# Kernel optimization log

Hardware: AMD Instinct MI355X
Metric: run time of the kernel (lower is better)

## Reference

```python
import jax, jax.numpy as jnp
import numpy as np
import math

FEATURE_DIM = 128
CLASS_NUM = 10000
BATCH = 4096


def setup_inputs() -> dict:
    key = jax.random.key(0)
    k1, k2, k3 = jax.random.split(key, 3)
    # feat scaled by 0.1 so squared distances are O(1) and exp(-d/1.8) is non-degenerate
    feat = jax.random.normal(k1, (BATCH, FEATURE_DIM), dtype=jnp.float32) * 0.1
    # xavier_uniform over [class_num, feature_dim]
    bound = math.sqrt(6.0 / (CLASS_NUM + FEATURE_DIM))
    weights = jax.random.uniform(k2, (CLASS_NUM, FEATURE_DIM), dtype=jnp.float32,
                                 minval=-bound, maxval=bound)
    label = jax.random.randint(k3, (BATCH,), 0, CLASS_NUM, dtype=jnp.int64)
    return {"feat": feat, "weights": weights, "label": label}


def reference(feat, weights, label):
    # pairwise squared euclidean distance via GEMM trick (avoids [B,C,D] diff tensor)
    f2 = jnp.sum(feat * feat, axis=-1, keepdims=True)          # [B,1]
    w2 = jnp.sum(weights * weights, axis=-1)[None, :]          # [1,C]
    metric = jnp.maximum(f2 + w2 - 2.0 * (feat @ weights.T), 0.0)  # [B,C]
    kernal_metric = jnp.exp(-metric / 1.8)                     # [B,C]
    # per-sample gather of the true-class kernel value; mean; clamp at 0.5
    cor = jnp.take_along_axis(kernal_metric, label[:, None].astype(jnp.int32), axis=1)[:, 0]
    avg = jnp.maximum(jnp.mean(cor), 0.5)
    # original uses .item() per sample -> scale is detached from the graph
    scale = jax.lax.stop_gradient(1.0 / avg) * math.log(CLASS_NUM - 1.0)
    return scale * kernal_metric
```

## Files before the change

### kernel.cpp

```cpp
#include <hip/hip_runtime.h>
#include <hip/hip_bf16.h>
#include <math.h>

#define FDIM  128
#define BATCH 4096
#define CNUM  10000

typedef __attribute__((ext_vector_type(8))) short short8;
typedef __attribute__((ext_vector_type(4))) float f32x4;

#define WS_FEATB 0
#define WS_WB    1048576
#define WS_F2    3608576
#define WS_W2    3624960
#define WS_COR   3664960

#define C2 0.80178372573096f

#define CGCLS 640

#define GL2LDS(g, l) __builtin_amdgcn_global_load_lds(                      \
    (const __attribute__((address_space(1))) void*)(g),                     \
    (__attribute__((address_space(3))) void*)(l), 16, 0, 0)

__global__ void prep_cor_kernel(const float* __restrict__ feat,
                                const float* __restrict__ weights,
                                const int* __restrict__ label,
                                __hip_bfloat16* __restrict__ featb,
                                __hip_bfloat16* __restrict__ wb,
                                float* __restrict__ f2,
                                float* __restrict__ w2,
                                float* __restrict__ cor) {
    int gw   = (blockIdx.x * blockDim.x + threadIdx.x) >> 6;
    int lane = threadIdx.x & 63;
    if (gw < BATCH + CNUM) {
        const float* src;
        __hip_bfloat16* dst;
        float* nrm;
        if (gw < BATCH) { src = feat    + (size_t)gw * FDIM; dst = featb + (size_t)gw * FDIM; nrm = f2 + gw; }
        else            { int r = gw - BATCH;
                          src = weights + (size_t)r  * FDIM; dst = wb    + (size_t)r  * FDIM; nrm = w2 + r; }
        float2 v = ((const float2*)src)[lane];
        __hip_bfloat162 b2;
        b2.x = __float2bfloat16(v.x);
        b2.y = __float2bfloat16(v.y);
        ((__hip_bfloat162*)dst)[lane] = b2;
        float ss = v.x * v.x + v.y * v.y;
        #pragma unroll
        for (int off = 32; off; off >>= 1) ss += __shfl_down(ss, off, 64);
        if (lane == 0) *nrm = ss;
    } else {
        int s = gw - (BATCH + CNUM);
        if (s >= BATCH) return;
        int lab = label[s];
        float2 f = ((const float2*)(feat    + (size_t)s   * FDIM))[lane];
        float2 w = ((const float2*)(weights + (size_t)lab * FDIM))[lane];
        float dx = f.x - w.x, dy = f.y - w.y;
        float ss = dx * dx + dy * dy;
        #pragma unroll
        for (int off = 32; off; off >>= 1) ss += __shfl_down(ss, off, 64);
        if (lane == 0) cor[s] = __expf(-ss * (1.0f / 1.8f));
    }
}

__launch_bounds__(512, 4)
__global__ void gemm_kernel(const __hip_bfloat16* __restrict__ featb,
                            const __hip_bfloat16* __restrict__ wb,
                            const float* __restrict__ f2,
                            const float* __restrict__ w2,
                            const float* __restrict__ cor,
                            float* __restrict__ out) {
    __shared__ __align__(16) char lds[65536];
    __shared__ __align__(16) float w2l[CGCLS];
    __shared__ float red[8];

    int bx   = blockIdx.x;
    int band = bx & 31;
    int cg   = bx >> 5;
    int tid  = threadIdx.x;
    int wid  = tid >> 6;
    int lane = tid & 63;
    int r16  = lane & 15;
    int kh   = lane >> 4;
    int aoff = (wid & 1) * 64;
    int boff = (wid >> 1) * 32;

    const char* Ab = (const char*)wb;
    const char* Bb = (const char*)featb;

    #pragma unroll
    for (int p = 0; p < 4; ++p) {
        int idx = tid + p * 512;
        int row = idx >> 4, chk = idx & 15;
        int gc = cg * CGCLS + row; gc = gc < CNUM ? gc : CNUM - 1;
        GL2LDS(Ab + (size_t)gc * 256 + (chk ^ (row & 7)) * 16, lds + idx * 16);
    }
    {
        float s = 0.0f;
        #pragma unroll
        for (int i = 0; i < BATCH / 512; ++i) s += cor[tid + i * 512];
        #pragma unroll
        for (int off = 32; off; off >>= 1) s += __shfl_down(s, off, 64);
        if (lane == 0) red[wid] = s;
    }
    #pragma unroll
    for (int p = 0; p < 2; ++p) {
        int idx = tid + p * 512;
        if (idx < CGCLS) {
            int cls = cg * CGCLS + idx;
            w2l[idx] = (cls < CNUM) ? w2[cls] : 0.0f;
        }
    }
    float f2n[2];
    short8 bfrag[4][2];
    #pragma unroll
    for (int n = 0; n < 2; ++n) {
        int rowg = band * 128 + boff + n * 16 + r16;
        f2n[n] = f2[rowg];
        #pragma unroll
        for (int kk = 0; kk < 4; ++kk)
            bfrag[kk][n] = *(const short8*)(Bb + (size_t)rowg * 256 + kk * 64 + kh * 16);
    }
    __syncthreads();

    float tot = 0.0f;
    #pragma unroll
    for (int i = 0; i < 8; ++i) tot += red[i];
    float avg = fmaxf(tot * (1.0f / BATCH), 0.5f);
    float ls2 = log2f(logf((float)(CNUM - 1)) / avg);

    #pragma unroll
    for (int it = 0; it < 5; ++it) {
        int cur = it & 1;

        if (it < 4) {
            #pragma unroll
            for (int p = 0; p < 4; ++p) {
                int idx = tid + p * 512;
                int row = idx >> 4, chk = idx & 15;
                int gc = cg * CGCLS + (it + 1) * 128 + row;
                gc = gc < CNUM ? gc : CNUM - 1;
                GL2LDS(Ab + (size_t)gc * 256 + (chk ^ (row & 7)) * 16,
                       lds + (cur ^ 1) * 32768 + idx * 16);
            }
        }
        __builtin_amdgcn_sched_barrier(0);

        const char* Abuf = lds + cur * 32768;

        #pragma unroll
        for (int mp = 0; mp < 2; ++mp) {
            f32x4 acc[2][2];
            #pragma unroll
            for (int mm = 0; mm < 2; ++mm)
                #pragma unroll
                for (int n = 0; n < 2; ++n) acc[mm][n] = (f32x4){0.f, 0.f, 0.f, 0.f};

            #pragma unroll
            for (int kk = 0; kk < 4; ++kk) {
                short8 a0, a1;
                {
                    int row0 = aoff + (mp * 2 + 0) * 16 + r16;
                    int c0 = (kk * 4 + kh) ^ (row0 & 7);
                    a0 = *(const short8*)(Abuf + row0 * 256 + c0 * 16);
                    int row1 = aoff + (mp * 2 + 1) * 16 + r16;
                    int c1 = (kk * 4 + kh) ^ (row1 & 7);
                    a1 = *(const short8*)(Abuf + row1 * 256 + c1 * 16);
                }
                #pragma unroll
                for (int n = 0; n < 2; ++n) {
                    acc[0][n] = __builtin_amdgcn_mfma_f32_16x16x32_bf16(a0, bfrag[kk][n], acc[0][n], 0, 0, 0);
                    acc[1][n] = __builtin_amdgcn_mfma_f32_16x16x32_bf16(a1, bfrag[kk][n], acc[1][n], 0, 0, 0);
                }
            }

            #pragma unroll
            for (int mm = 0; mm < 2; ++mm) {
                int lcl = it * 128 + aoff + (mp * 2 + mm) * 16 + kh * 4;
                int cm0 = cg * CGCLS + lcl;
                bool ok = cm0 < CNUM;
                f32x4 w4 = *(const f32x4*)(&w2l[lcl]);
                #pragma unroll
                for (int n = 0; n < 2; ++n) {
                    f32x4 v;
                    #pragma unroll
                    for (int r = 0; r < 4; ++r) {
                        float mt2 = fmaf(-2.0f, acc[mm][n][r], f2n[n] + w4[r]);
                        mt2 = fmaxf(mt2, 0.0f);
                        v[r] = exp2f(fmaf(mt2, -C2, ls2));
                    }
                    if (ok) {
                        size_t rg = (size_t)(band * 128 + boff + n * 16 + r16);
                        *(f32x4*)(out + rg * CNUM + cm0) = v;
                    }
                }
            }
        }

        asm volatile("s_waitcnt vmcnt(8)" ::: "memory");
        __builtin_amdgcn_sched_barrier(0);
        __builtin_amdgcn_s_barrier();
    }
}

extern "C" void kernel_launch(void* const* d_in, const int* in_sizes, int n_in,
                              void* d_out, int out_size, void* d_ws, size_t ws_size,
                              hipStream_t stream) {
    (void)in_sizes; (void)n_in; (void)out_size; (void)ws_size;
    const float* feat    = (const float*)d_in[0];
    const float* weights = (const float*)d_in[1];
    const int*   label   = (const int*)d_in[2];
    float* out = (float*)d_out;
    char*  ws  = (char*)d_ws;

    __hip_bfloat16* featb = (__hip_bfloat16*)(ws + WS_FEATB);
    __hip_bfloat16* wb    = (__hip_bfloat16*)(ws + WS_WB);
    float* f2  = (float*)(ws + WS_F2);
    float* w2  = (float*)(ws + WS_W2);
    float* cor = (float*)(ws + WS_COR);

    const int total_waves = BATCH + CNUM + BATCH;
    prep_cor_kernel<<<(total_waves + 3) / 4, 256, 0, stream>>>(
        feat, weights, label, featb, wb, f2, w2, cor);

    gemm_kernel<<<512, 512, 0, stream>>>(featb, wb, f2, w2, cor, out);
}
```

Measured before the change: 47.49 us.

## Retile GEMM to 64-row bands with 1280-class groups and paired output stores

Changes the block tile from 128 batch rows x 640 classes to 64 batch rows x 1280 classes, with 8 waves arranged 4x2, so each wave now computes a 32x32 sub-tile per 128-class step across 10 steps. Epilogue results from even steps are held in registers and written together with the odd step's results, batching global stores. The intent is to halve weight-tile reloads per class group relative to feature rows and to group stores into larger bursts. In exchange it holds more live registers, and even steps now wait on vmcnt(0), which may stall the prefetch pipeline.

```diff
diff --git a/kernel.cpp b/kernel.cpp
--- a/kernel.cpp
+++ b/kernel.cpp
@@ -17,7 +17,7 @@
 
 #define C2 0.80178372573096f
 
-#define CGCLS 640
+#define CGCLS 1280
 
 #define GL2LDS(g, l) __builtin_amdgcn_global_load_lds(                      \
     (const __attribute__((address_space(1))) void*)(g),                     \
@@ -75,15 +75,15 @@
     __shared__ float red[8];
 
     int bx   = blockIdx.x;
-    int band = bx & 31;
-    int cg   = bx >> 5;
+    int band = bx & 63;
+    int cg   = bx >> 6;
     int tid  = threadIdx.x;
     int wid  = tid >> 6;
     int lane = tid & 63;
     int r16  = lane & 15;
     int kh   = lane >> 4;
-    int aoff = (wid & 1) * 64;
-    int boff = (wid >> 1) * 32;
+    int aoff = (wid & 3) * 32;
+    int boff = (wid >> 2) * 32;
 
     const char* Ab = (const char*)wb;
     const char* Bb = (const char*)featb;
@@ -104,7 +104,7 @@
         if (lane == 0) red[wid] = s;
     }
     #pragma unroll
-    for (int p = 0; p < 2; ++p) {
+    for (int p = 0; p < 3; ++p) {
         int idx = tid + p * 512;
         if (idx < CGCLS) {
             int cls = cg * CGCLS + idx;
@@ -115,7 +115,7 @@
     short8 bfrag[4][2];
     #pragma unroll
     for (int n = 0; n < 2; ++n) {
-        int rowg = band * 128 + boff + n * 16 + r16;
+        int rowg = band * 64 + boff + n * 16 + r16;
         f2n[n] = f2[rowg];
         #pragma unroll
         for (int kk = 0; kk < 4; ++kk)
@@ -129,16 +129,18 @@
     float avg = fmaxf(tot * (1.0f / BATCH), 0.5f);
     float ls2 = log2f(logf((float)(CNUM - 1)) / avg);
 
-    #pragma unroll
-    for (int it = 0; it < 5; ++it) {
-        int cur = it & 1;
-
-        if (it < 4) {
+    f32x4 hold[2][2];
+
+    #pragma unroll
+    for (int t = 0; t < 10; ++t) {
+        int cur = t & 1;
+
+        if (t < 9) {
             #pragma unroll
             for (int p = 0; p < 4; ++p) {
                 int idx = tid + p * 512;
                 int row = idx >> 4, chk = idx & 15;
-                int gc = cg * CGCLS + (it + 1) * 128 + row;
+                int gc = cg * CGCLS + (t + 1) * 128 + row;
                 gc = gc < CNUM ? gc : CNUM - 1;
                 GL2LDS(Ab + (size_t)gc * 256 + (chk ^ (row & 7)) * 16,
                        lds + (cur ^ 1) * 32768 + idx * 16);
@@ -147,38 +149,31 @@
         __builtin_amdgcn_sched_barrier(0);
 
         const char* Abuf = lds + cur * 32768;
-
-        #pragma unroll
-        for (int mp = 0; mp < 2; ++mp) {
-            f32x4 acc[2][2];
+        f32x4 acc[2][2];
+        #pragma unroll
+        for (int mm = 0; mm < 2; ++mm)
+            #pragma unroll
+            for (int n = 0; n < 2; ++n) acc[mm][n] = (f32x4){0.f, 0.f, 0.f, 0.f};
+        #pragma unroll
+        for (int kk = 0; kk < 4; ++kk) {
+            short8 a[2];
+            #pragma unroll
+            for (int mm = 0; mm < 2; ++mm) {
+                int row = aoff + mm * 16 + r16;
+                int c = (kk * 4 + kh) ^ (row & 7);
+                a[mm] = *(const short8*)(Abuf + row * 256 + c * 16);
+            }
             #pragma unroll
             for (int mm = 0; mm < 2; ++mm)
                 #pragma unroll
-                for (int n = 0; n < 2; ++n) acc[mm][n] = (f32x4){0.f, 0.f, 0.f, 0.f};
-
-            #pragma unroll
-            for (int kk = 0; kk < 4; ++kk) {
-                short8 a0, a1;
-                {
-                    int row0 = aoff + (mp * 2 + 0) * 16 + r16;
-                    int c0 = (kk * 4 + kh) ^ (row0 & 7);
-                    a0 = *(const short8*)(Abuf + row0 * 256 + c0 * 16);
-                    int row1 = aoff + (mp * 2 + 1) * 16 + r16;
-                    int c1 = (kk * 4 + kh) ^ (row1 & 7);
-                    a1 = *(const short8*)(Abuf + row1 * 256 + c1 * 16);
-                }
-                #pragma unroll
-                for (int n = 0; n < 2; ++n) {
-                    acc[0][n] = __builtin_amdgcn_mfma_f32_16x16x32_bf16(a0, bfrag[kk][n], acc[0][n], 0, 0, 0);
-                    acc[1][n] = __builtin_amdgcn_mfma_f32_16x16x32_bf16(a1, bfrag[kk][n], acc[1][n], 0, 0, 0);
-                }
-            }
-
-            #pragma unroll
-            for (int mm = 0; mm < 2; ++mm) {
-                int lcl = it * 128 + aoff + (mp * 2 + mm) * 16 + kh * 4;
-                int cm0 = cg * CGCLS + lcl;
-                bool ok = cm0 < CNUM;
+                for (int n = 0; n < 2; ++n)
+                    acc[mm][n] = __builtin_amdgcn_mfma_f32_16x16x32_bf16(a[mm], bfrag[kk][n], acc[mm][n], 0, 0, 0);
+        }
+
+        if ((t & 1) == 0) {
+            #pragma unroll
+            for (int mm = 0; mm < 2; ++mm) {
+                int lcl = t * 128 + aoff + mm * 16 + kh * 4;
                 f32x4 w4 = *(const f32x4*)(&w2l[lcl]);
                 #pragma unroll
                 for (int n = 0; n < 2; ++n) {
@@ -189,17 +184,54 @@
                         mt2 = fmaxf(mt2, 0.0f);
                         v[r] = exp2f(fmaf(mt2, -C2, ls2));
                     }
+                    hold[mm][n] = v;
+                }
+            }
+        } else {
+            #pragma unroll
+            for (int mm = 0; mm < 2; ++mm) {
+                int cm0 = cg * CGCLS + (t - 1) * 128 + aoff + mm * 16 + kh * 4;
+                bool ok = cm0 < CNUM;
+                #pragma unroll
+                for (int n = 0; n < 2; ++n) {
                     if (ok) {
-                        size_t rg = (size_t)(band * 128 + boff + n * 16 + r16);
+                        size_t rg = (size_t)(band * 64 + boff + n * 16 + r16);
+                        *(f32x4*)(out + rg * CNUM + cm0) = hold[mm][n];
+                    }
+                }
+            }
+            #pragma unroll
+            for (int mm = 0; mm < 2; ++mm) {
+                int lcl = t * 128 + aoff + mm * 16 + kh * 4;
+                int cm0 = cg * CGCLS + lcl;
+                bool ok = cm0 < CNUM;
+                f32x4 w4 = *(const f32x4*)(&w2l[lcl]);
+                #pragma unroll
+                for (int n = 0; n < 2; ++n) {
+                    f32x4 v;
+                    #pragma unroll
+                    for (int r = 0; r < 4; ++r) {
+                        float mt2 = fmaf(-2.0f, acc[mm][n][r], f2n[n] + w4[r]);
+                        mt2 = fmaxf(mt2, 0.0f);
+                        v[r] = exp2f(fmaf(mt2, -C2, ls2));
+                    }
+                    if (ok) {
+                        size_t rg = (size_t)(band * 64 + boff + n * 16 + r16);
                         *(f32x4*)(out + rg * CNUM + cm0) = v;
                     }
                 }
             }
         }
 
-        asm volatile("s_waitcnt vmcnt(8)" ::: "memory");
-        __builtin_amdgcn_sched_barrier(0);
-        __builtin_amdgcn_s_barrier();
+        if (t < 9) {
+            if ((t & 1) == 0) {
+                asm volatile("s_waitcnt vmcnt(0)" ::: "memory");
+            } else {
+                asm volatile("s_waitcnt vmcnt(8)" ::: "memory");
+            }
+            __builtin_amdgcn_sched_barrier(0);
+            __builtin_amdgcn_s_barrier();
+        }
     }
 }
 
```

Result: slower. 48.47 us (+2.1%).
